# Optimization experiments

Hardware: AMD Instinct MI355X
Metric: run time of the kernel (lower is better)

Reference implementation:

```python
import jax, jax.numpy as jnp
import numpy as np

B, T, D, A = 64, 1024, 768, 128

def setup_inputs() -> dict:
    key = jax.random.key(0)
    k1, k2, k3 = jax.random.split(key, 3)
    x = jax.random.normal(k1, (B, T, D), dtype=jnp.float32)
    # glorot_normal-style scaling for the learned projections
    W1 = jax.random.normal(k2, (D, A), dtype=jnp.float32) * np.sqrt(2.0 / (D + A))
    W2 = jax.random.normal(k3, (A, T), dtype=jnp.float32) * np.sqrt(2.0 / (A + T))
    return {"x": x, "W1": W1, "W2": W2}

def reference(x, W1, W2):
    # x: [B, T, D], W1: [D, A], W2: [A, T]
    OA = jnp.tanh(jnp.einsum('btd,da->bta', x, W1))      # [B, T, A]
    OA = jnp.einsum('bta,as->bts', OA, W2)               # [B, T, T]
    OA = jax.nn.softmax(OA, axis=-2)                     # softmax over source-time axis
    # ot[b,s,d] = sum_t x[b,t,d] * OA[b,t,s]  (x^T @ OA, then transpose back)
    ot = jnp.einsum('btd,bts->bsd', x, OA)               # [B, T, D]
    return ot
```

## Files before the change

### kernel.cpp

```cpp
#include <hip/hip_runtime.h>
#include <math.h>

#define B_ 64
#define T_ 1024
#define D_ 768
#define A_ 128

typedef __attribute__((ext_vector_type(4))) float f32x4;
typedef __attribute__((ext_vector_type(8))) short s16x8;
typedef __attribute__((ext_vector_type(4))) short s16x4;

__device__ inline short f2b(float f) {
  union { float f; unsigned u; } v; v.f = f;
  unsigned r = (v.u + 0x7FFFu + ((v.u >> 16) & 1u)) >> 16;
  return (short)r;
}
__device__ inline float b2f(short s) {
  union { unsigned u; float f; } v; v.u = ((unsigned)(unsigned short)s) << 16;
  return v.f;
}

__device__ inline void gll16(const void* g, const void* lds) {
  __builtin_amdgcn_global_load_lds(
      (const __attribute__((address_space(1))) unsigned*)g,
      (__attribute__((address_space(3))) unsigned*)lds, 16, 0, 0);
}

__global__ __launch_bounds__(512, 2)
void g4_div(const short* __restrict__ Ag, const short* __restrict__ Bg,
            const float* __restrict__ Rs, float* __restrict__ Cg) {
  __shared__ __align__(16) short AS[2][16384];
  __shared__ __align__(16) short BS[2][16384];
  unsigned nwg = gridDim.x;
  unsigned L = blockIdx.x;
  unsigned xcd = L & 7u, base = L >> 3;
  unsigned q = nwg >> 3, r = nwg & 7u;
  unsigned id = (xcd < r ? xcd * (q + 1) : r * (q + 1) + (xcd - r) * q) + base;
  const int bz = id / 12;
  const int rem = id - bz * 12;
  const int by = rem / 3, bx = rem - (rem / 3) * 3;
  const int m0 = by * 256, n0 = bx * 256;

  const short* Ab = Ag + (size_t)bz * (T_ * T_);
  const short* Bb = Bg + (size_t)bz * (D_ * T_);
  const float* rsb = Rs + (size_t)bz * T_;
  float* Cb = Cg + (size_t)bz * (T_ * D_);

  const int tid = threadIdx.x;
  const int w = tid >> 6, lane = tid & 63;
  const int wr = w >> 2, wc = w & 3;
  const int lr = lane & 15, lq = lane >> 4;
  const int swzk = (lane & 7) ^ ((lane >> 3) & 7);
  const int abase = (wr * 128 + lr) * 64;
  const int bbase = (wc * 64 + lr) * 64;
  const int sx = lr & 7;
  const int sl0 = (lq ^ sx) * 8;
  const int sl1 = ((4 + lq) ^ sx) * 8;

  f32x4 acc[8][4] = {};
  s16x8 bq[4][2];

#define STG(dst, src, r0, kt)                                                  \
  { _Pragma("unroll")                                                          \
    for (int jj = 0; jj < 2; ++jj) {                                           \
      int rr = jj * 64 + w * 8 + (lane >> 3);                                  \
      gll16((src) + (size_t)((r0) + rr) * 1024 + (kt) + swzk * 8,              \
            (dst) + jj * 4096 + w * 512);                                      \
    } }

#define PH2(P, Q0, VM, ...)                                                    \
  {                                                                            \
    s16x8 a0_ = *(const s16x8*)&AS[P][abase + (2 * (Q0)) * 1024 + sl0];        \
    s16x8 a1_ = *(const s16x8*)&AS[P][abase + (2 * (Q0)) * 1024 + sl1];        \
    s16x8 a2_ = *(const s16x8*)&AS[P][abase + (2 * (Q0) + 1) * 1024 + sl0];    \
    s16x8 a3_ = *(const s16x8*)&AS[P][abase + (2 * (Q0) + 1) * 1024 + sl1];    \
    if ((Q0) == 0) {                                                           \
      _Pragma("unroll")                                                        \
      for (int nf = 0; nf < 4; ++nf) {                                         \
        bq[nf][0] = *(const s16x8*)&BS[P][bbase + nf * 1024 + sl0];            \
        bq[nf][1] = *(const s16x8*)&BS[P][bbase + nf * 1024 + sl1];            \
      }                                                                        \
    }                                                                          \
    __VA_ARGS__;                                                               \
    VM;                                                                        \
    __builtin_amdgcn_s_barrier();                                              \
    asm volatile("s_waitcnt lgkmcnt(0)" ::: "memory");                         \
    __builtin_amdgcn_s_setprio(1);                                             \
    _Pragma("unroll")                                                          \
    for (int nf = 0; nf < 4; ++nf) {                                           \
      acc[2*(Q0)][nf]   = __builtin_amdgcn_mfma_f32_16x16x32_bf16(a0_, bq[nf][0], acc[2*(Q0)][nf], 0, 0, 0);   \
      acc[2*(Q0)+1][nf] = __builtin_amdgcn_mfma_f32_16x16x32_bf16(a2_, bq[nf][0], acc[2*(Q0)+1][nf], 0, 0, 0); \
    }                                                                          \
    s16x8 a4_ = *(const s16x8*)&AS[P][abase + (2 * (Q0) + 2) * 1024 + sl0];    \
    s16x8 a5_ = *(const s16x8*)&AS[P][abase + (2 * (Q0) + 2) * 1024 + sl1];    \
    s16x8 a6_ = *(const s16x8*)&AS[P][abase + (2 * (Q0) + 3) * 1024 + sl0];    \
    s16x8 a7_ = *(const s16x8*)&AS[P][abase + (2 * (Q0) + 3) * 1024 + sl1];    \
    _Pragma("unroll")                                                          \
    for (int nf = 0; nf < 4; ++nf) {                                           \
      acc[2*(Q0)][nf]   = __builtin_amdgcn_mfma_f32_16x16x32_bf16(a1_, bq[nf][1], acc[2*(Q0)][nf], 0, 0, 0);   \
      acc[2*(Q0)+1][nf] = __builtin_amdgcn_mfma_f32_16x16x32_bf16(a3_, bq[nf][1], acc[2*(Q0)+1][nf], 0, 0, 0); \
    }                                                                          \
    _Pragma("unroll")                                                          \
    for (int nf = 0; nf < 4; ++nf) {                                           \
      acc[2*(Q0)+2][nf] = __builtin_amdgcn_mfma_f32_16x16x32_bf16(a4_, bq[nf][0], acc[2*(Q0)+2][nf], 0, 0, 0); \
      acc[2*(Q0)+3][nf] = __builtin_amdgcn_mfma_f32_16x16x32_bf16(a6_, bq[nf][0], acc[2*(Q0)+3][nf], 0, 0, 0); \
    }                                                                          \
    _Pragma("unroll")                                                          \
    for (int nf = 0; nf < 4; ++nf) {                                           \
      acc[2*(Q0)+2][nf] = __builtin_amdgcn_mfma_f32_16x16x32_bf16(a5_, bq[nf][1], acc[2*(Q0)+2][nf], 0, 0, 0); \
      acc[2*(Q0)+3][nf] = __builtin_amdgcn_mfma_f32_16x16x32_bf16(a7_, bq[nf][1], acc[2*(Q0)+3][nf], 0, 0, 0); \
    }                                                                          \
    __builtin_amdgcn_s_setprio(0);                                             \
    __builtin_amdgcn_s_barrier();                                              \
  }

#define VM4 asm volatile("s_waitcnt vmcnt(4)" ::: "memory")
#define VM0 asm volatile("s_waitcnt vmcnt(0)" ::: "memory")
#define NOP (void)0

  STG(&BS[0][0],    Bb, n0,       0);
  STG(&BS[0][8192], Bb, n0 + 128, 0);
  STG(&AS[0][0],    Ab, m0,       0);
  STG(&AS[0][8192], Ab, m0 + 128, 0);
  STG(&BS[1][0],    Bb, n0,       64);
  STG(&BS[1][8192], Bb, n0 + 128, 64);
  VM4;
  __builtin_amdgcn_s_barrier();

  for (int j = 0; j < 7; ++j) {
    const int kb = j * 128;
    PH2(0, 0, NOP,
        STG(&AS[1][0],    Ab, m0,       kb + 64);
        STG(&AS[1][8192], Ab, m0 + 128, kb + 64));
    PH2(0, 2, VM4,
        STG(&BS[0][0],    Bb, n0,       kb + 128);
        STG(&BS[0][8192], Bb, n0 + 128, kb + 128));
    PH2(1, 0, NOP,
        STG(&AS[0][0],    Ab, m0,       kb + 128);
        STG(&AS[0][8192], Ab, m0 + 128, kb + 128));
    PH2(1, 2, VM4,
        STG(&BS[1][0],    Bb, n0,       kb + 192);
        STG(&BS[1][8192], Bb, n0 + 128, kb + 192));
  }
  PH2(0, 0, NOP,
      STG(&AS[1][0],    Ab, m0,       960);
      STG(&AS[1][8192], Ab, m0 + 128, 960));
  PH2(0, 2, VM0, NOP);
  PH2(1, 0, NOP, NOP);
  PH2(1, 2, NOP, NOP);

#undef STG
#undef PH2
#undef VM4
#undef VM0
#undef NOP

#pragma unroll
  for (int mf = 0; mf < 8; ++mf) {
    f32x4 rsv = *(const f32x4*)&rsb[m0 + wr * 128 + mf * 16 + lq * 4];
    f32x4 inv;
#pragma unroll
    for (int qq = 0; qq < 4; ++qq) {
      float iv;
      asm("v_rcp_f32 %0, %1" : "=v"(iv) : "v"(rsv[qq]));
      inv[qq] = iv;
    }
#pragma unroll
    for (int nf = 0; nf < 4; ++nf) {
      int m = m0 + wr * 128 + mf * 16 + lq * 4;
      int n = n0 + wc * 64 + nf * 16 + lr;
#pragma unroll
      for (int qq = 0; qq < 4; ++qq)
        Cb[(size_t)(m + qq) * D_ + n] = acc[mf][nf][qq] * inv[qq];
    }
  }
}

__global__ __launch_bounds__(512, 4)
void g12(const short* __restrict__ W1tg, const float* __restrict__ xg,
         const short* __restrict__ W2tg, short* __restrict__ Stg,
         float* __restrict__ rsg, short* __restrict__ xtg, int nb) {
  __shared__ __align__(16) short SMEM[33792];
  short* As = SMEM;
  short* Bs = SMEM + 8192;
  short* Ts = SMEM + 16384;
  short* Hs = SMEM;
  short* B2 = SMEM + 16384;

  unsigned nwg = gridDim.x;
  unsigned L = blockIdx.x;
  unsigned xcd = L & 7u, base = L >> 3;
  unsigned q = nwg >> 3, r = nwg & 7u;
  unsigned id = (xcd < r ? xcd * (q + 1) : r * (q + 1) + (xcd - r) * q) + base;
  const int bz = id >> 3, bt = id & 7;
  const int t0 = bt * 128;

  const float* xb = xg + (size_t)bz * T_ * D_;
  short* Xtb = xtg + (size_t)bz * ((size_t)D_ * T_);
  short* Stb = Stg + (size_t)bz * (T_ * T_);
  float* rsb = rsg + (size_t)bz * T_;

  const int tid = threadIdx.x;
  const int w = tid >> 6, lane = tid & 63;
  const int wva = w >> 2, wvt = w & 3;
  const int lr = lane & 15, lq = lane >> 4;
  const int swzk = (lane & 7) ^ ((lane >> 3) & 7);
  const int sxl = lr & 7;
  const int sl0 = (lq ^ sxl) * 8;
  const int sl1 = ((4 + lq) ^ sxl) * 8;

  f32x4 acc[4][2] = {};

  float4 xf0[2], xf1[2];
#pragma unroll
  for (int u = 0; u < 2; ++u) {
    int c = tid * 2 + u;
    int row = c >> 3, k8 = c & 7;
    const float* gp = xb + (size_t)(t0 + row) * D_ + k8 * 8;
    xf0[u] = *(const float4*)gp;
    xf1[u] = *(const float4*)(gp + 4);
  }

  for (int k0 = 0; k0 < D_; k0 += 64) {
    __syncthreads();
#pragma unroll
    for (int u = 0; u < 2; ++u) {
      int c = tid * 2 + u;
      int row = c >> 3, k8 = c & 7;
      s16x8 p;
      p[0] = f2b(xf0[u].x); p[1] = f2b(xf0[u].y);
      p[2] = f2b(xf0[u].z); p[3] = f2b(xf0[u].w);
      p[4] = f2b(xf1[u].x); p[5] = f2b(xf1[u].y);
      p[6] = f2b(xf1[u].z); p[7] = f2b(xf1[u].w);
      *(s16x8*)&Bs[row * 64 + ((k8 ^ (row & 7)) << 3)] = p;
#pragma unroll
      for (int j = 0; j < 8; ++j) {
        int d = k8 * 8 + j;
        Ts[d * 136 + (row ^ (d & 32))] = p[j];
      }
    }
#pragma unroll
    for (int i = 0; i < 2; ++i) {
      int chunk = w * 2 + i;
      int row = chunk * 8 + (lane >> 3);
      gll16(W1tg + (size_t)row * D_ + k0 + swzk * 8, As + chunk * 512);
    }
    __syncthreads();
    if (k0 + 64 < D_) {
#pragma unroll
      for (int u = 0; u < 2; ++u) {
        int c = tid * 2 + u;
        int row = c >> 3, k8 = c & 7;
        const float* gp = xb + (size_t)(t0 + row) * D_ + (k0 + 64) + k8 * 8;
        xf0[u] = *(const float4*)gp;
        xf1[u] = *(const float4*)(gp + 4);
      }
    }
#pragma unroll
    for (int kk = 0; kk < 2; ++kk) {
      const int sl = kk ? sl1 : sl0;
      s16x8 a[4], b[2];
#pragma unroll
      for (int mf = 0; mf < 4; ++mf)
        a[mf] = *(const s16x8*)&As[(wva * 64 + mf * 16 + lr) * 64 + sl];
#pragma unroll
      for (int nf = 0; nf < 2; ++nf)
        b[nf] = *(const s16x8*)&Bs[(wvt * 32 + nf * 16 + lr) * 64 + sl];
#pragma unroll
      for (int mf = 0; mf < 4; ++mf)
#pragma unroll
        for (int nf = 0; nf < 2; ++nf)
          acc[mf][nf] = __builtin_amdgcn_mfma_f32_16x16x32_bf16(
              a[mf], b[nf], acc[mf][nf], 0, 0, 0);
    }
#pragma unroll
    for (int u = 0; u < 2; ++u) {
      int task = tid + u * 512;
      int dd = task >> 4, t8 = task & 15;
      *(s16x8*)&Xtb[(size_t)(k0 + dd) * T_ + t0 + t8 * 8] =
          *(const s16x8*)&Ts[dd * 136 + ((t8 ^ ((dd >> 3) & 4)) << 3)];
    }
  }

  __syncthreads();
#pragma unroll
  for (int mf = 0; mf < 4; ++mf)
#pragma unroll
    for (int nf = 0; nf < 2; ++nf) {
      int ml = wva * 64 + mf * 16 + lq * 4;
      int nl = wvt * 32 + nf * 16 + lr;
      s16x4 pk;
#pragma unroll
      for (int qq = 0; qq < 4; ++qq) pk[qq] = f2b(tanhf(acc[mf][nf][qq]));
      int slot = (ml >> 3) ^ (nl & 7);
      *(s16x4*)&Hs[nl * 128 + (slot << 3) + (ml & 7)] = pk;
    }
  __syncthreads();

  const int wvt2 = w >> 2, wvs = w & 3;
  for (int si = 0; si < 8; ++si) {
    const int s0 = si * 128;
#pragma unroll
    for (int i = 0; i < 4; ++i) {
      int c = w * 4 + i;
      int row = 4 * c + (lane >> 4);
      gll16(W2tg + (size_t)(s0 + row) * A_ + (((lane & 15) ^ (row & 7)) << 3),
            B2 + c * 512);
    }
    __syncthreads();
    f32x4 ac2[4][2] = {};
#pragma unroll
    for (int kk = 0; kk < 4; ++kk) {
      s16x8 a[4], b[2];
#pragma unroll
      for (int mf = 0; mf < 4; ++mf) {
        int row = wvt2 * 64 + mf * 16 + lr;
        a[mf] = *(const s16x8*)&Hs[row * 128 + (((kk * 4 + lq) ^ sxl) << 3)];
      }
#pragma unroll
      for (int nf = 0; nf < 2; ++nf) {
        int row = wvs * 32 + nf * 16 + lr;
        b[nf] = *(const s16x8*)&B2[row * 128 + (((kk * 4 + lq) ^ sxl) << 3)];
      }
#pragma unroll
      for (int mf = 0; mf < 4; ++mf)
#pragma unroll
        for (int nf = 0; nf < 2; ++nf)
          ac2[mf][nf] = __builtin_amdgcn_mfma_f32_16x16x32_bf16(
              a[mf], b[nf], ac2[mf][nf], 0, 0, 0);
    }
    __syncthreads();
    float psum[2] = {0.f, 0.f};
#pragma unroll
    for (int mf = 0; mf < 4; ++mf)
#pragma unroll
      for (int nf = 0; nf < 2; ++nf) {
        int ml = wvt2 * 64 + mf * 16 + lq * 4;
        int nl = wvs * 32 + nf * 16 + lr;
        s16x4 pk;
#pragma unroll
        for (int qq = 0; qq < 4; ++qq) {
          float v = __expf(ac2[mf][nf][qq]);
          pk[qq] = f2b(v);
          psum[nf] += b2f(pk[qq]);
        }
        *(s16x4*)&B2[nl * 136 + ml] = pk;
      }
#pragma unroll
    for (int nf = 0; nf < 2; ++nf) {
      psum[nf] += __shfl_xor(psum[nf], 16);
      psum[nf] += __shfl_xor(psum[nf], 32);
    }
    if (lq == 0) {
#pragma unroll
      for (int nf = 0; nf < 2; ++nf)
        atomicAdd(&rsb[s0 + wvs * 32 + nf * 16 + lr], psum[nf]);
    }
    __syncthreads();
#pragma unroll
    for (int it = 0; it < 4; ++it) {
      int row = it * 32 + (tid >> 4);
      int col = (tid & 15) * 8;
      *(s16x8*)&Stb[(size_t)(s0 + row) * T_ + t0 + col] =
          *(const s16x8*)&B2[row * 136 + col];
    }
    __syncthreads();
  }
}

__global__ __launch_bounds__(256)
void transpose_cvt(const float* __restrict__ src, short* __restrict__ dst,
                   int R, int C) {
  __shared__ float sh[64][65];
  const int tid = threadIdx.x;
  const float* s = src + (size_t)blockIdx.z * R * C;
  short* d = dst + (size_t)blockIdx.z * R * C;
  const int r0 = blockIdx.y * 64, c0 = blockIdx.x * 64;
#pragma unroll
  for (int u = 0; u < 4; ++u) {
    int e = tid + u * 256;
    int rr = e >> 4, cc4 = (e & 15) * 4;
    float4 v = *(const float4*)&s[(size_t)(r0 + rr) * C + c0 + cc4];
    sh[rr][cc4 + 0] = v.x;
    sh[rr][cc4 + 1] = v.y;
    sh[rr][cc4 + 2] = v.z;
    sh[rr][cc4 + 3] = v.w;
  }
  __syncthreads();
#pragma unroll
  for (int u = 0; u < 4; ++u) {
    int e = tid + u * 256;
    int dr = e >> 4, tc4 = (e & 15) * 4;
    s16x4 pk;
#pragma unroll
    for (int j = 0; j < 4; ++j) pk[j] = f2b(sh[tc4 + j][dr]);
    *(s16x4*)&d[(size_t)(c0 + dr) * R + r0 + tc4] = pk;
  }
}

extern "C" void kernel_launch(void* const* d_in, const int* in_sizes, int n_in,
                              void* d_out, int out_size, void* d_ws, size_t ws_size,
                              hipStream_t stream) {
  const float* x  = (const float*)d_in[0];
  const float* W1 = (const float*)d_in[1];
  const float* W2 = (const float*)d_in[2];
  float* out = (float*)d_out;

  short* xt  = (short*)d_ws;
  short* W1t = xt + (size_t)B_ * D_ * T_;
  short* W2t = W1t + (size_t)A_ * D_;
  float* rs  = (float*)(W2t + (size_t)T_ * A_);
  short* St  = (short*)(rs + (size_t)B_ * T_);
  size_t fixed_bytes = (size_t)((char*)St - (char*)xt);
  long avail = (long)ws_size - (long)fixed_bytes;
  long per_b = (long)T_ * T_ * sizeof(short);
  int chunk = (int)(avail > 0 ? avail / per_b : 0);
  if (chunk > B_) chunk = B_;
  if (chunk < 1) chunk = 1;

  hipMemsetAsync(rs, 0, (size_t)B_ * T_ * sizeof(float), stream);

  transpose_cvt<<<dim3(A_ / 64, D_ / 64, 1), 256, 0, stream>>>(W1, W1t, D_, A_);
  transpose_cvt<<<dim3(T_ / 64, A_ / 64, 1), 256, 0, stream>>>(W2, W2t, A_, T_);

  for (int b0 = 0; b0 < B_; b0 += chunk) {
    int nb = B_ - b0; if (nb > chunk) nb = chunk;
    g12<<<8 * nb, 512, 0, stream>>>(
        W1t, x + (size_t)b0 * T_ * D_, W2t, St,
        rs + (size_t)b0 * T_, xt + (size_t)b0 * (size_t)D_ * T_, nb);
    g4_div<<<12 * nb, 512, 0, stream>>>(
        St, xt + (size_t)b0 * (size_t)D_ * T_, rs + (size_t)b0 * T_,
        out + (size_t)b0 * (size_t)T_ * D_);
  }
}
```

Before: 250.5 us.

## Load W1/W2 fragments directly to registers and double-buffer LDS in g12

In the fused projection kernel, the W1 and W2 operand tiles are now read straight from global memory into MFMA fragment registers instead of being staged through LDS with global_load_lds. The x-tile staging buffers (B and transposed tiles) are double-buffered so each k-iteration needs only one barrier. __syncthreads is replaced by raw s_barrier plus explicit lgkmcnt waits. The aim is fewer barriers and less LDS traffic, at the cost of uncoalesced per-lane global loads of the weights and more register pressure.

```diff
diff --git a/kernel.cpp b/kernel.cpp
--- a/kernel.cpp
+++ b/kernel.cpp
@@ -25,6 +25,9 @@
       (const __attribute__((address_space(1))) unsigned*)g,
       (__attribute__((address_space(3))) unsigned*)lds, 16, 0, 0);
 }
+
+#define LGKM0 asm volatile("s_waitcnt lgkmcnt(0)" ::: "memory")
+#define RBAR  { __builtin_amdgcn_s_barrier(); asm volatile("" ::: "memory"); }
 
 __global__ __launch_bounds__(512, 2)
 void g4_div(const short* __restrict__ Ag, const short* __restrict__ Bg,
@@ -181,11 +184,8 @@
          const short* __restrict__ W2tg, short* __restrict__ Stg,
          float* __restrict__ rsg, short* __restrict__ xtg, int nb) {
   __shared__ __align__(16) short SMEM[33792];
-  short* As = SMEM;
-  short* Bs = SMEM + 8192;
-  short* Ts = SMEM + 16384;
   short* Hs = SMEM;
-  short* B2 = SMEM + 16384;
+  short* Bb = SMEM + 16384;
 
   unsigned nwg = gridDim.x;
   unsigned L = blockIdx.x;
@@ -204,7 +204,6 @@
   const int w = tid >> 6, lane = tid & 63;
   const int wva = w >> 2, wvt = w & 3;
   const int lr = lane & 15, lq = lane >> 4;
-  const int swzk = (lane & 7) ^ ((lane >> 3) & 7);
   const int sxl = lr & 7;
   const int sl0 = (lq ^ sxl) * 8;
   const int sl1 = ((4 + lq) ^ sxl) * 8;
@@ -221,8 +220,18 @@
     xf1[u] = *(const float4*)(gp + 4);
   }
 
-  for (int k0 = 0; k0 < D_; k0 += 64) {
-    __syncthreads();
+  for (int it = 0; it < 12; ++it) {
+    const int k0 = it * 64;
+    short* BsC = SMEM + (it & 1) * 8192;
+    short* TsC = SMEM + 16384 + (it & 1) * 8704;
+
+    s16x8 a0[4], a1[4];
+#pragma unroll
+    for (int mf = 0; mf < 4; ++mf) {
+      const short* wp = W1tg + (size_t)(wva * 64 + mf * 16 + lr) * D_ + k0;
+      a0[mf] = *(const s16x8*)(wp + lq * 8);
+      a1[mf] = *(const s16x8*)(wp + 32 + lq * 8);
+    }
 #pragma unroll
     for (int u = 0; u < 2; ++u) {
       int c = tid * 2 + u;
@@ -232,21 +241,14 @@
       p[2] = f2b(xf0[u].z); p[3] = f2b(xf0[u].w);
       p[4] = f2b(xf1[u].x); p[5] = f2b(xf1[u].y);
       p[6] = f2b(xf1[u].z); p[7] = f2b(xf1[u].w);
-      *(s16x8*)&Bs[row * 64 + ((k8 ^ (row & 7)) << 3)] = p;
+      *(s16x8*)&BsC[row * 64 + ((k8 ^ (row & 7)) << 3)] = p;
 #pragma unroll
       for (int j = 0; j < 8; ++j) {
         int d = k8 * 8 + j;
-        Ts[d * 136 + (row ^ (d & 32))] = p[j];
+        TsC[d * 136 + (row ^ (d & 32))] = p[j];
       }
     }
-#pragma unroll
-    for (int i = 0; i < 2; ++i) {
-      int chunk = w * 2 + i;
-      int row = chunk * 8 + (lane >> 3);
-      gll16(W1tg + (size_t)row * D_ + k0 + swzk * 8, As + chunk * 512);
-    }
-    __syncthreads();
-    if (k0 + 64 < D_) {
+    if (it < 11) {
 #pragma unroll
       for (int u = 0; u < 2; ++u) {
         int c = tid * 2 + u;
@@ -256,33 +258,31 @@
         xf1[u] = *(const float4*)(gp + 4);
       }
     }
-#pragma unroll
-    for (int kk = 0; kk < 2; ++kk) {
-      const int sl = kk ? sl1 : sl0;
-      s16x8 a[4], b[2];
-#pragma unroll
-      for (int mf = 0; mf < 4; ++mf)
-        a[mf] = *(const s16x8*)&As[(wva * 64 + mf * 16 + lr) * 64 + sl];
-#pragma unroll
-      for (int nf = 0; nf < 2; ++nf)
-        b[nf] = *(const s16x8*)&Bs[(wvt * 32 + nf * 16 + lr) * 64 + sl];
-#pragma unroll
-      for (int mf = 0; mf < 4; ++mf)
-#pragma unroll
-        for (int nf = 0; nf < 2; ++nf)
-          acc[mf][nf] = __builtin_amdgcn_mfma_f32_16x16x32_bf16(
-              a[mf], b[nf], acc[mf][nf], 0, 0, 0);
-    }
+    LGKM0; RBAR;
 #pragma unroll
     for (int u = 0; u < 2; ++u) {
       int task = tid + u * 512;
       int dd = task >> 4, t8 = task & 15;
       *(s16x8*)&Xtb[(size_t)(k0 + dd) * T_ + t0 + t8 * 8] =
-          *(const s16x8*)&Ts[dd * 136 + ((t8 ^ ((dd >> 3) & 4)) << 3)];
-    }
-  }
-
-  __syncthreads();
+          *(const s16x8*)&TsC[dd * 136 + ((t8 ^ ((dd >> 3) & 4)) << 3)];
+    }
+#pragma unroll
+    for (int kk = 0; kk < 2; ++kk) {
+      const int sl = kk ? sl1 : sl0;
+      s16x8 b[2];
+#pragma unroll
+      for (int nf = 0; nf < 2; ++nf)
+        b[nf] = *(const s16x8*)&BsC[(wvt * 32 + nf * 16 + lr) * 64 + sl];
+#pragma unroll
+      for (int mf = 0; mf < 4; ++mf)
+#pragma unroll
+        for (int nf = 0; nf < 2; ++nf)
+          acc[mf][nf] = __builtin_amdgcn_mfma_f32_16x16x32_bf16(
+              kk ? a1[mf] : a0[mf], b[nf], acc[mf][nf], 0, 0, 0);
+    }
+  }
+
+  RBAR;
 #pragma unroll
   for (int mf = 0; mf < 4; ++mf)
 #pragma unroll
@@ -295,76 +295,74 @@
       int slot = (ml >> 3) ^ (nl & 7);
       *(s16x4*)&Hs[nl * 128 + (slot << 3) + (ml & 7)] = pk;
     }
-  __syncthreads();
+  LGKM0; RBAR;
 
   const int wvt2 = w >> 2, wvs = w & 3;
   for (int si = 0; si < 8; ++si) {
     const int s0 = si * 128;
-#pragma unroll
-    for (int i = 0; i < 4; ++i) {
-      int c = w * 4 + i;
-      int row = 4 * c + (lane >> 4);
-      gll16(W2tg + (size_t)(s0 + row) * A_ + (((lane & 15) ^ (row & 7)) << 3),
-            B2 + c * 512);
-    }
-    __syncthreads();
+    s16x8 bfr[4][2];
+#pragma unroll
+    for (int kk = 0; kk < 4; ++kk)
+#pragma unroll
+      for (int nf = 0; nf < 2; ++nf)
+        bfr[kk][nf] = *(const s16x8*)&W2tg[
+            (size_t)(s0 + wvs * 32 + nf * 16 + lr) * A_ + kk * 32 + lq * 8];
     f32x4 ac2[4][2] = {};
 #pragma unroll
     for (int kk = 0; kk < 4; ++kk) {
-      s16x8 a[4], b[2];
+      s16x8 a[4];
 #pragma unroll
       for (int mf = 0; mf < 4; ++mf) {
         int row = wvt2 * 64 + mf * 16 + lr;
         a[mf] = *(const s16x8*)&Hs[row * 128 + (((kk * 4 + lq) ^ sxl) << 3)];
       }
 #pragma unroll
-      for (int nf = 0; nf < 2; ++nf) {
-        int row = wvs * 32 + nf * 16 + lr;
-        b[nf] = *(const s16x8*)&B2[row * 128 + (((kk * 4 + lq) ^ sxl) << 3)];
-      }
-#pragma unroll
       for (int mf = 0; mf < 4; ++mf)
 #pragma unroll
         for (int nf = 0; nf < 2; ++nf)
           ac2[mf][nf] = __builtin_amdgcn_mfma_f32_16x16x32_bf16(
-              a[mf], b[nf], ac2[mf][nf], 0, 0, 0);
-    }
-    __syncthreads();
+              a[mf], bfr[kk][nf], ac2[mf][nf], 0, 0, 0);
+    }
     float psum[2] = {0.f, 0.f};
+    s16x4 pkk[4][2];
+#pragma unroll
+    for (int mf = 0; mf < 4; ++mf)
+#pragma unroll
+      for (int nf = 0; nf < 2; ++nf) {
+#pragma unroll
+        for (int qq = 0; qq < 4; ++qq) {
+          float v = __expf(ac2[mf][nf][qq]);
+          pkk[mf][nf][qq] = f2b(v);
+          psum[nf] += b2f(pkk[mf][nf][qq]);
+        }
+      }
+#pragma unroll
+    for (int nf = 0; nf < 2; ++nf) {
+      psum[nf] += __shfl_xor(psum[nf], 16);
+      psum[nf] += __shfl_xor(psum[nf], 32);
+    }
+    if (lq == 0) {
+#pragma unroll
+      for (int nf = 0; nf < 2; ++nf)
+        atomicAdd(&rsb[s0 + wvs * 32 + nf * 16 + lr], psum[nf]);
+    }
+    RBAR;
 #pragma unroll
     for (int mf = 0; mf < 4; ++mf)
 #pragma unroll
       for (int nf = 0; nf < 2; ++nf) {
         int ml = wvt2 * 64 + mf * 16 + lq * 4;
         int nl = wvs * 32 + nf * 16 + lr;
-        s16x4 pk;
-#pragma unroll
-        for (int qq = 0; qq < 4; ++qq) {
-          float v = __expf(ac2[mf][nf][qq]);
-          pk[qq] = f2b(v);
-          psum[nf] += b2f(pk[qq]);
-        }
-        *(s16x4*)&B2[nl * 136 + ml] = pk;
+        *(s16x4*)&Bb[nl * 136 + ml] = pkk[mf][nf];
       }
-#pragma unroll
-    for (int nf = 0; nf < 2; ++nf) {
-      psum[nf] += __shfl_xor(psum[nf], 16);
-      psum[nf] += __shfl_xor(psum[nf], 32);
-    }
-    if (lq == 0) {
-#pragma unroll
-      for (int nf = 0; nf < 2; ++nf)
-        atomicAdd(&rsb[s0 + wvs * 32 + nf * 16 + lr], psum[nf]);
-    }
-    __syncthreads();
-#pragma unroll
-    for (int it = 0; it < 4; ++it) {
-      int row = it * 32 + (tid >> 4);
+    LGKM0; RBAR;
+#pragma unroll
+    for (int itc = 0; itc < 4; ++itc) {
+      int row = itc * 32 + (tid >> 4);
       int col = (tid & 15) * 8;
       *(s16x8*)&Stb[(size_t)(s0 + row) * T_ + t0 + col] =
-          *(const s16x8*)&B2[row * 136 + col];
-    }
-    __syncthreads();
+          *(const s16x8*)&Bb[row * 136 + col];
+    }
   }
 }
 
```

New measurement: 268.0 us. 1.07x slower.

## Split fused projection kernel into separate tanh-projection and score kernels

Applied to the files above, without the earlier changes.

The fused g12 kernel is split into g1k, which computes tanh(x@W1), writes H to a global bf16 buffer and emits transposed x, and g2k, which reloads H via global_load_lds and computes the H@W2 scores plus row sums. The split lowers LDS use in the first stage (25600 shorts instead of 33792) and lets each kernel use its own registers and occupancy. The cost is an extra launch and a round trip of H through global memory.

```diff
diff --git a/kernel.cpp b/kernel.cpp
--- a/kernel.cpp
+++ b/kernel.cpp
@@ -177,15 +177,12 @@
 }
 
 __global__ __launch_bounds__(512, 4)
-void g12(const short* __restrict__ W1tg, const float* __restrict__ xg,
-         const short* __restrict__ W2tg, short* __restrict__ Stg,
-         float* __restrict__ rsg, short* __restrict__ xtg, int nb) {
-  __shared__ __align__(16) short SMEM[33792];
+void g1k(const short* __restrict__ W1tg, const float* __restrict__ xg,
+         short* __restrict__ Hgg, short* __restrict__ xtg) {
+  __shared__ __align__(16) short SMEM[25600];
   short* As = SMEM;
   short* Bs = SMEM + 8192;
   short* Ts = SMEM + 16384;
-  short* Hs = SMEM;
-  short* B2 = SMEM + 16384;
 
   unsigned nwg = gridDim.x;
   unsigned L = blockIdx.x;
@@ -197,8 +194,7 @@
 
   const float* xb = xg + (size_t)bz * T_ * D_;
   short* Xtb = xtg + (size_t)bz * ((size_t)D_ * T_);
-  short* Stb = Stg + (size_t)bz * (T_ * T_);
-  float* rsb = rsg + (size_t)bz * T_;
+  short* Hgb = Hgg + (size_t)bz * (T_ * A_);
 
   const int tid = threadIdx.x;
   const int w = tid >> 6, lane = tid & 63;
@@ -292,9 +288,49 @@
       s16x4 pk;
 #pragma unroll
       for (int qq = 0; qq < 4; ++qq) pk[qq] = f2b(tanhf(acc[mf][nf][qq]));
-      int slot = (ml >> 3) ^ (nl & 7);
-      *(s16x4*)&Hs[nl * 128 + (slot << 3) + (ml & 7)] = pk;
-    }
+      *(s16x4*)&SMEM[nl * 136 + ml] = pk;
+    }
+  __syncthreads();
+#pragma unroll
+  for (int u = 0; u < 4; ++u) {
+    int task = tid + u * 512;
+    int row = task >> 4, c8 = task & 15;
+    *(s16x8*)&Hgb[(size_t)(t0 + row) * A_ + c8 * 8] =
+        *(const s16x8*)&SMEM[row * 136 + c8 * 8];
+  }
+}
+
+__global__ __launch_bounds__(512, 4)
+void g2k(const short* __restrict__ Hgg, const short* __restrict__ W2tg,
+         short* __restrict__ Stg, float* __restrict__ rsg) {
+  __shared__ __align__(16) short SMEM[33792];
+  short* Hs = SMEM;
+  short* B2 = SMEM + 16384;
+
+  unsigned nwg = gridDim.x;
+  unsigned L = blockIdx.x;
+  unsigned xcd = L & 7u, base = L >> 3;
+  unsigned q = nwg >> 3, r = nwg & 7u;
+  unsigned id = (xcd < r ? xcd * (q + 1) : r * (q + 1) + (xcd - r) * q) + base;
+  const int bz = id >> 3, bt = id & 7;
+  const int t0 = bt * 128;
+
+  const short* Hgb = Hgg + (size_t)bz * (T_ * A_);
+  short* Stb = Stg + (size_t)bz * (T_ * T_);
+  float* rsb = rsg + (size_t)bz * T_;
+
+  const int tid = threadIdx.x;
+  const int w = tid >> 6, lane = tid & 63;
+  const int lr = lane & 15, lq = lane >> 4;
+  const int sxl = lr & 7;
+
+#pragma unroll
+  for (int i = 0; i < 4; ++i) {
+    int c = w * 4 + i;
+    int row = 4 * c + (lane >> 4);
+    gll16(Hgb + (size_t)(t0 + row) * A_ + (((lane & 15) ^ (row & 7)) << 3),
+          Hs + c * 512);
+  }
   __syncthreads();
 
   const int wvt2 = w >> 2, wvs = w & 3;
@@ -409,7 +445,8 @@
   short* xt  = (short*)d_ws;
   short* W1t = xt + (size_t)B_ * D_ * T_;
   short* W2t = W1t + (size_t)A_ * D_;
-  float* rs  = (float*)(W2t + (size_t)T_ * A_);
+  short* Hg  = W2t + (size_t)T_ * A_;
+  float* rs  = (float*)(Hg + (size_t)B_ * T_ * A_);
   short* St  = (short*)(rs + (size_t)B_ * T_);
   size_t fixed_bytes = (size_t)((char*)St - (char*)xt);
   long avail = (long)ws_size - (long)fixed_bytes;
@@ -425,9 +462,11 @@
 
   for (int b0 = 0; b0 < B_; b0 += chunk) {
     int nb = B_ - b0; if (nb > chunk) nb = chunk;
-    g12<<<8 * nb, 512, 0, stream>>>(
-        W1t, x + (size_t)b0 * T_ * D_, W2t, St,
-        rs + (size_t)b0 * T_, xt + (size_t)b0 * (size_t)D_ * T_, nb);
+    g1k<<<8 * nb, 512, 0, stream>>>(
+        W1t, x + (size_t)b0 * T_ * D_,
+        Hg + (size_t)b0 * T_ * A_, xt + (size_t)b0 * (size_t)D_ * T_);
+    g2k<<<8 * nb, 512, 0, stream>>>(
+        Hg + (size_t)b0 * T_ * A_, W2t, St, rs + (size_t)b0 * T_);
     g4_div<<<12 * nb, 512, 0, stream>>>(
         St, xt + (size_t)b0 * (size_t)D_ * T_, rs + (size_t)b0 * T_,
         out + (size_t)b0 * (size_t)T_ * D_);
```

New measurement: 261.2 us. 4.3% more time.
